# Performance work log

Hardware: AMD Instinct MI355X
Metric: run time of the kernel (lower is better)

Reference implementation:

```python
import jax, jax.numpy as jnp
import numpy as np

B, L, W = 4096, 30, 5          # batch, MAX_TOKEN_LENGTH, WINDOW_SIZE
A, E = 30, 128                 # ALPHABET_SIZE, embedding dim
C = 40                         # OUT_CHANNELS
H, T = 128, 3                  # LSTM_UNITS, num CRF tags
LIN = W * C                    # 200
EPS = 1e-5


def setup_inputs():
    key = jax.random.key(0)
    ks = jax.random.split(key, 24)
    def rn(k, shape, s=0.1):
        return jax.random.normal(k, shape, jnp.float32) * s
    return {
        'x': jax.random.randint(ks[0], (B, L, W), 0, A, jnp.int32),
        'emb': rn(ks[1], (A, E), 1.0),
        'conv_w': rn(ks[2], (C, E, 3)),
        'conv_b': rn(ks[3], (C,)),
        'bn1_g': 1.0 + rn(ks[4], (C,)),
        'bn1_b': rn(ks[5], (C,)),
        'bn1_m': rn(ks[6], (C,)),
        'bn1_v': 0.5 + jax.random.uniform(ks[7], (C,), jnp.float32),
        'w_ih_f': rn(ks[8], (4 * H, LIN)),
        'w_hh_f': rn(ks[9], (4 * H, H)),
        'b_f': rn(ks[10], (4 * H,)),
        'w_ih_b': rn(ks[11], (4 * H, LIN)),
        'w_hh_b': rn(ks[12], (4 * H, H)),
        'b_b': rn(ks[13], (4 * H,)),
        'bn2_g': 1.0 + rn(ks[14], (2 * H,)),
        'bn2_b': rn(ks[15], (2 * H,)),
        'bn2_m': rn(ks[16], (2 * H,)),
        'bn2_v': 0.5 + jax.random.uniform(ks[17], (2 * H,), jnp.float32),
        'fc_w': rn(ks[18], (T, 2 * H)),
        'fc_b': rn(ks[19], (T,)),
        'trans': rn(ks[20], (T, T)),
        'start_t': rn(ks[21], (T,)),
        'end_t': rn(ks[22], (T,)),
    }


def _lstm_dir(seq, w_ih, w_hh, b, reverse):
    # seq: [B, L, F]; torch gate order i, f, g, o
    xs = jnp.einsum('blf,gf->lbg', seq, w_ih) + b  # [L, B, 4H]
    h0 = jnp.zeros((seq.shape[0], H), seq.dtype)
    def step(carry, xt):
        h, c = carry
        z = xt + h @ w_hh.T
        i, f, g, o = jnp.split(z, 4, axis=-1)
        c = jax.nn.sigmoid(f) * c + jax.nn.sigmoid(i) * jnp.tanh(g)
        h = jax.nn.sigmoid(o) * jnp.tanh(c)
        return (h, c), h
    _, hs = jax.lax.scan(step, (h0, h0), xs, reverse=reverse)
    return hs.transpose(1, 0, 2)  # [B, L, H]


def _viterbi(emis, mask, trans, start_t, end_t):
    # emis: [B, L, T], mask: [B, L] bool
    score = start_t + emis[:, 0]                      # [B, T]
    def step(score, inp):
        e_t, m_t = inp                                # [B, T], [B]
        cand = score[:, :, None] + trans              # [B, Tprev, Tnext]
        ptr = jnp.argmax(cand, axis=1)                # [B, T]
        new = jnp.max(cand, axis=1) + e_t
        return jnp.where(m_t[:, None], new, score), ptr
    score, hist = jax.lax.scan(
        step, score, (emis[:, 1:].transpose(1, 0, 2), mask[:, 1:].T))
    score = score + end_t
    best = jnp.max(score, axis=1)                     # [B] path scores
    last = jnp.argmax(score, axis=1)                  # [B]
    def back(tag, inp):
        h_t, m_t = inp
        prev = jnp.take_along_axis(h_t, tag[:, None], axis=1)[:, 0]
        tag = jnp.where(m_t, prev, tag)
        return tag, tag
    _, ys = jax.lax.scan(back, last, (hist, mask[:, 1:].T), reverse=True)
    tags = jnp.concatenate([ys, last[None]], axis=0).T  # [B, L]
    return best, tags


def reference(x, emb, conv_w, conv_b, bn1_g, bn1_b, bn1_m, bn1_v,
              w_ih_f, w_hh_f, b_f, w_ih_b, w_hh_b, b_b,
              bn2_g, bn2_b, bn2_m, bn2_v, fc_w, fc_b, trans, start_t, end_t):
    mask = x[:, :, 2] > 0                             # [B, L]
    e = emb[x.reshape(B * L, W)]                      # [N, W, E]  (dropout=eval noop)
    e = e.transpose(0, 2, 1)                          # [N, E, W]
    y = jax.lax.conv_general_dilated(
        e, conv_w, (1,), [(1, 1)],
        dimension_numbers=('NCH', 'OIH', 'NCH')) + conv_b[:, None]
    # BatchNorm1d (inference, running stats)
    y = (y - bn1_m[:, None]) * (bn1_g / jnp.sqrt(bn1_v + EPS))[:, None] + bn1_b[:, None]
    y = jax.nn.relu(y)
    # MaxPool1d(k=3, stride=1, pad=1): length preserved
    y = jax.lax.reduce_window(y, -jnp.inf, jax.lax.max,
                              (1, 1, 3), (1, 1, 1),
                              [(0, 0), (0, 0), (1, 1)])
    y = y.reshape(B, L, LIN)                          # torch.flatten is channel-major = row-major reshape
    hf = _lstm_dir(y, w_ih_f, w_hh_f, b_f, False)
    hb = _lstm_dir(y, w_ih_b, w_hh_b, b_b, True)
    h = jnp.concatenate([hf, hb], axis=-1)            # [B, L, 2H]
    h = (h - bn2_m) * (bn2_g / jnp.sqrt(bn2_v + EPS)) + bn2_b
    emis = h @ fc_w.T + fc_b                          # [B, L, T]
    return _viterbi(emis, mask, trans, start_t, end_t)
```

## Files before the change

kernel.cpp:

```cpp
#include <hip/hip_runtime.h>
#include <math.h>

#define BB    4096
#define LL    30
#define WW    5
#define CC    40
#define HH    128
#define TT    3
#define KA    328
#define NB    32
#define NT_   512
#define FSTR  232
#define HSTR  136
#define CW    1056

#define WS_P    0
#define WS_BC   3600
#define WS_BG   3648
#define WS_WFC  4672
#define WS_EB   5440
#define WS_WBF  5504
#define WS_EMIS (5504 + 540672)

typedef __bf16 bf16x8 __attribute__((ext_vector_type(8)));
typedef float  f32x4  __attribute__((ext_vector_type(4)));
typedef unsigned short u16x8 __attribute__((ext_vector_type(8)));

__device__ __forceinline__ float sigm(float x) {
    return __builtin_amdgcn_rcpf(1.0f + __expf(-x));
}
__device__ __forceinline__ float tanh_fast(float x) {
    return 2.0f * __builtin_amdgcn_rcpf(1.0f + __expf(-2.0f * x)) - 1.0f;
}
__device__ __forceinline__ unsigned short f2bf(float f) {
    unsigned u = __builtin_bit_cast(unsigned, f);
    return (unsigned short)((u + 0x7FFFu + ((u >> 16) & 1u)) >> 16);
}
__device__ __forceinline__ float bf2f(unsigned short h) {
    unsigned u = ((unsigned)h) << 16;
    return __builtin_bit_cast(float, u);
}

__global__ void prep_kernel(const float* __restrict__ emb, const float* __restrict__ conv_w,
                            const float* __restrict__ conv_b,
                            const float* __restrict__ bn1_g, const float* __restrict__ bn1_b,
                            const float* __restrict__ bn1_m, const float* __restrict__ bn1_v,
                            const float* __restrict__ w_ih_f, const float* __restrict__ w_hh_f,
                            const float* __restrict__ b_f,
                            const float* __restrict__ w_ih_b, const float* __restrict__ w_hh_b,
                            const float* __restrict__ b_b,
                            const float* __restrict__ bn2_g, const float* __restrict__ bn2_b,
                            const float* __restrict__ bn2_m, const float* __restrict__ bn2_v,
                            const float* __restrict__ fc_w, const float* __restrict__ fc_b,
                            float* __restrict__ ws)
{
    const int gid = blockIdx.x * blockDim.x + threadIdx.x;
    const int gsz = gridDim.x * blockDim.x;

    for (int idx = gid; idx < 3600; idx += gsz) {
        int k = idx / 1200, rem = idx % 1200, a = rem / 40, c = rem % 40;
        float s1 = bn1_g[c] / sqrtf(bn1_v[c] + 1e-5f);
        float acc = 0.f;
        for (int e = 0; e < 128; ++e)
            acc += emb[a * 128 + e] * conv_w[(c * 128 + e) * 3 + k];
        ws[WS_P + idx] = acc * s1;
    }
    for (int c = gid; c < CC; c += gsz) {
        float s1 = bn1_g[c] / sqrtf(bn1_v[c] + 1e-5f);
        ws[WS_BC + c] = (conv_b[c] - bn1_m[c]) * s1 + bn1_b[c];
    }
    for (int i = gid; i < 1024; i += gsz) {
        int d = i >> 9, g = i & 511;
        ws[WS_BG + i] = d ? b_b[g] : b_f[g];
    }
    for (int i = gid; i < 768; i += gsz) {
        int d = i / 384, r = i % 384, t = r / 128, u = r % 128;
        int j = d * 128 + u;
        float s2 = bn2_g[j] / sqrtf(bn2_v[j] + 1e-5f);
        ws[WS_WFC + i] = fc_w[t * 256 + j] * s2;
    }
    for (int t = gid; t < TT; t += gsz) {
        float acc = fc_b[t];
        for (int j = 0; j < 256; ++j) {
            float s2 = bn2_g[j] / sqrtf(bn2_v[j] + 1e-5f);
            acc += fc_w[t * 256 + j] * (bn2_b[j] - bn2_m[j] * s2);
        }
        ws[WS_EB + t] = acc;
    }
    unsigned short* wsu = (unsigned short*)ws;
    for (int i = gid; i < 2 * 512 * CW; i += gsz) {
        int d = i / (512 * CW), r = i % (512 * CW);
        int n = r / CW, q = r % CW;
        int Ks = q / 96, t = q % 96, s = t / 32, k32 = t % 32;
        int k = Ks * 32 + k32;
        int u = n >> 2, g = n & 3, row = g * 128 + u;
        const float* wih = d ? w_ih_b : w_ih_f;
        const float* whh = d ? w_hh_b : w_hh_f;
        float w = (k < 200) ? wih[row * 200 + k]
                            : ((k >= 224) ? whh[row * 128 + (k - 224)] : 0.f);
        unsigned short t0 = f2bf(w);
        float r1 = w - bf2f(t0);
        unsigned short t1 = f2bf(r1);
        unsigned short t2 = f2bf(r1 - bf2f(t1));
        wsu[2 * WS_WBF + i] = (s == 0) ? t0 : ((s == 1) ? t1 : t2);
    }
}

__global__ __launch_bounds__(512, 2)
void lstm_kernel(const int* __restrict__ x, float* __restrict__ ws)
{
    __shared__ unsigned short Fh[2][NB * FSTR], Fl[2][NB * FSTR], Fm[2][NB * FSTR];
    __shared__ unsigned short Hh[2][NB * HSTR], Hl[2][NB * HSTR], Hm[2][NB * HSTR];
    __shared__ float Pp_s[3600];
    __shared__ float Wfc_s[384];
    __shared__ float biasC_s[40];

    const int tid = threadIdx.x;
    const int d   = blockIdx.x & 1;
    const int b0  = (blockIdx.x >> 1) * NB;

    const unsigned short* __restrict__ Wb =
        (const unsigned short*)ws + 2 * WS_WBF + d * (512 * CW);
    float* emis = ws + WS_EMIS + d * (BB * LL * TT);

    for (int i = tid; i < 3600; i += NT_) Pp_s[i] = ws[WS_P + i];
    for (int i = tid; i < 384;  i += NT_) Wfc_s[i] = ws[WS_WFC + d * 384 + i];
    for (int i = tid; i < 40;   i += NT_) biasC_s[i] = ws[WS_BC + i];
    for (int i = tid; i < NB * FSTR; i += NT_) {
        ((unsigned*)Fh)[i] = 0u; ((unsigned*)Fl)[i] = 0u; ((unsigned*)Fm)[i] = 0u;
    }
    for (int i = tid; i < NB * HSTR; i += NT_) {
        ((unsigned*)Hh)[i] = 0u; ((unsigned*)Hl)[i] = 0u; ((unsigned*)Hm)[i] = 0u;
    }

    const int lane = tid & 63;
    const int wv   = tid >> 6;
    const int quad = lane >> 4;
    const int ml   = lane & 15;
    const int skey = (wv ^ (wv >> 2)) & 1;

    const unsigned short* __restrict__ Wn[4] = {
        Wb + (wv * 64 +  0 + ml) * CW + quad * 8,
        Wb + (wv * 64 + 16 + ml) * CW + quad * 8,
        Wb + (wv * 64 + 32 + ml) * CW + quad * 8,
        Wb + (wv * 64 + 48 + ml) * CW + quad * 8
    };

    const float* bgp = ws + WS_BG + d * 512;
    int   un[4];
    float bIv[4], bFv[4], bGv[4], bOv[4];
    #pragma unroll
    for (int nt = 0; nt < 4; ++nt) {
        int u = wv * 16 + nt * 4 + quad;
        un[nt]  = u;
        bIv[nt] = bgp[u];
        bFv[nt] = bgp[128 + u];
        bGv[nt] = bgp[256 + u];
        bOv[nt] = bgp[384 + u];
    }

    float cst[2][4];
    #pragma unroll
    for (int mt = 0; mt < 2; ++mt)
        #pragma unroll
        for (int nt = 0; nt < 4; ++nt) cst[mt][nt] = 0.f;

    __syncthreads();

#define FEAT_ONE(LPOS, BUF, P)                                                 \
    {                                                                          \
        int bb = (P) / CC, c = (P) % CC;                                       \
        const int* tok = x + (((b0 + bb) * LL) + (LPOS)) * WW;                 \
        int t0 = tok[0], t1 = tok[1], t2 = tok[2], t3 = tok[3], t4 = tok[4];   \
        float bc = biasC_s[c];                                                 \
        float a0 = bc + Pp_s[(30 + t0) * 40 + c] + Pp_s[(60 + t1) * 40 + c];   \
        float a1 = bc + Pp_s[t0 * 40 + c] + Pp_s[(30 + t1) * 40 + c] + Pp_s[(60 + t2) * 40 + c]; \
        float a2 = bc + Pp_s[t1 * 40 + c] + Pp_s[(30 + t2) * 40 + c] + Pp_s[(60 + t3) * 40 + c]; \
        float a3 = bc + Pp_s[t2 * 40 + c] + Pp_s[(30 + t3) * 40 + c] + Pp_s[(60 + t4) * 40 + c]; \
        float a4 = bc + Pp_s[t3 * 40 + c] + Pp_s[(30 + t4) * 40 + c];          \
        a0 = fmaxf(a0, 0.f); a1 = fmaxf(a1, 0.f); a2 = fmaxf(a2, 0.f);         \
        a3 = fmaxf(a3, 0.f); a4 = fmaxf(a4, 0.f);                              \
        float f[5];                                                            \
        f[0] = fmaxf(a0, a1);                                                  \
        f[1] = fmaxf(fmaxf(a0, a1), a2);                                       \
        f[2] = fmaxf(fmaxf(a1, a2), a3);                                       \
        f[3] = fmaxf(fmaxf(a2, a3), a4);                                       \
        f[4] = fmaxf(a3, a4);                                                  \
        int base = bb * FSTR + c * 5;                                          \
        _Pragma("unroll")                                                      \
        for (int j = 0; j < 5; ++j) {                                          \
            unsigned short h0 = f2bf(f[j]);                                    \
            float r1 = f[j] - bf2f(h0);                                        \
            unsigned short h1 = f2bf(r1);                                      \
            unsigned short h2 = f2bf(r1 - bf2f(h1));                           \
            Fh[BUF][base + j] = h0;                                            \
            Fl[BUF][base + j] = h1;                                            \
            Fm[BUF][base + j] = h2;                                            \
        }                                                                      \
    }

#define FEAT_ITEMS(LPOS, BUF)                                                  \
    {                                                                          \
        FEAT_ONE(LPOS, BUF, tid)                                               \
        if (tid >= 192) FEAT_ONE(LPOS, BUF, tid + 320)                         \
        if (tid >= 192) FEAT_ONE(LPOS, BUF, tid + 640)                         \
        if (tid >= 384) FEAT_ONE(LPOS, BUF, tid + 768)                         \
    }

#define EMIS_BODY(LPOS, HB)                                                    \
    {                                                                          \
        int bb = tid / 6, r6 = tid % 6, t = r6 >> 1, seg = r6 & 1;             \
        int hoff = bb * HSTR + seg * 64;                                       \
        const float* wfc = &Wfc_s[t * 128 + seg * 64];                         \
        float s = 0.f;                                                         \
        _Pragma("unroll")                                                      \
        for (int i = 0; i < 8; ++i) {                                          \
            u16x8 v0 = *(const u16x8*)&Hh[HB][hoff + i * 8];                   \
            u16x8 v1 = *(const u16x8*)&Hl[HB][hoff + i * 8];                   \
            u16x8 v2 = *(const u16x8*)&Hm[HB][hoff + i * 8];                   \
            _Pragma("unroll")                                                  \
            for (int j = 0; j < 8; ++j) {                                      \
                float h = bf2f(v0[j]) + bf2f(v1[j]) + bf2f(v2[j]);             \
                s += h * wfc[i * 8 + j];                                       \
            }                                                                  \
        }                                                                      \
        s += __shfl_xor(s, 1);                                                 \
        if (seg == 0)                                                          \
            emis[(((b0 + bb) * LL) + (LPOS)) * TT + t] = s;                    \
    }

#define SHADOW_WORK(STEP_, FBN)                                                \
    {                                                                          \
        if ((STEP_) + 1 < LL) {                                                \
            const int lnext = d ? (LL - 2 - (STEP_)) : ((STEP_) + 1);          \
            FEAT_ITEMS(lnext, FBN)                                             \
        }                                                                      \
        if ((STEP_) > 0 && tid < 192) {                                        \
            const int lprev = d ? (LL - (STEP_)) : ((STEP_) - 1);              \
            EMIS_BODY(lprev, hr)                                               \
        }                                                                      \
    }

    {
        const int l0 = d ? (LL - 1) : 0;
        FEAT_ITEMS(l0, 0)
    }

#define WLOAD(B, P, KS)                                                        \
        {                                                                      \
            B[0] = *(const bf16x8*)((P) + (KS) * 96);                          \
            B[1] = *(const bf16x8*)((P) + (KS) * 96 + 32);                     \
            B[2] = *(const bf16x8*)((P) + (KS) * 96 + 64);                     \
        }
#define LDA(BUF, KS)                                                           \
        {                                                                      \
            if ((KS) < 7) {                                                    \
                const int ko_ = (KS) * 32 + quad * 8;                          \
                ah[BUF][0] = *(const bf16x8*)&Fh[fb][ml * FSTR + ko_];         \
                al[BUF][0] = *(const bf16x8*)&Fl[fb][ml * FSTR + ko_];         \
                am[BUF][0] = *(const bf16x8*)&Fm[fb][ml * FSTR + ko_];         \
                ah[BUF][1] = *(const bf16x8*)&Fh[fb][(16 + ml) * FSTR + ko_];  \
                al[BUF][1] = *(const bf16x8*)&Fl[fb][(16 + ml) * FSTR + ko_];  \
                am[BUF][1] = *(const bf16x8*)&Fm[fb][(16 + ml) * FSTR + ko_];  \
            } else {                                                           \
                const int ko_ = ((KS) - 7) * 32 + quad * 8;                    \
                ah[BUF][0] = *(const bf16x8*)&Hh[hr][ml * HSTR + ko_];         \
                al[BUF][0] = *(const bf16x8*)&Hl[hr][ml * HSTR + ko_];         \
                am[BUF][0] = *(const bf16x8*)&Hm[hr][ml * HSTR + ko_];         \
                ah[BUF][1] = *(const bf16x8*)&Hh[hr][(16 + ml) * HSTR + ko_];  \
                al[BUF][1] = *(const bf16x8*)&Hl[hr][(16 + ml) * HSTR + ko_];  \
                am[BUF][1] = *(const bf16x8*)&Hm[hr][(16 + ml) * HSTR + ko_];  \
            }                                                                  \
        }
#define GEMM6X(B, CB, NT)                                                      \
        {                                                                      \
            acc[0][NT] = __builtin_amdgcn_mfma_f32_16x16x32_bf16(B[0], ah[CB][0], acc[0][NT], 0, 0, 0); \
            acc[0][NT] = __builtin_amdgcn_mfma_f32_16x16x32_bf16(B[0], al[CB][0], acc[0][NT], 0, 0, 0); \
            acc[0][NT] = __builtin_amdgcn_mfma_f32_16x16x32_bf16(B[1], ah[CB][0], acc[0][NT], 0, 0, 0); \
            acc[0][NT] = __builtin_amdgcn_mfma_f32_16x16x32_bf16(B[1], al[CB][0], acc[0][NT], 0, 0, 0); \
            acc[0][NT] = __builtin_amdgcn_mfma_f32_16x16x32_bf16(B[2], ah[CB][0], acc[0][NT], 0, 0, 0); \
            acc[0][NT] = __builtin_amdgcn_mfma_f32_16x16x32_bf16(B[0], am[CB][0], acc[0][NT], 0, 0, 0); \
            acc[1][NT] = __builtin_amdgcn_mfma_f32_16x16x32_bf16(B[0], ah[CB][1], acc[1][NT], 0, 0, 0); \
            acc[1][NT] = __builtin_amdgcn_mfma_f32_16x16x32_bf16(B[0], al[CB][1], acc[1][NT], 0, 0, 0); \
            acc[1][NT] = __builtin_amdgcn_mfma_f32_16x16x32_bf16(B[1], ah[CB][1], acc[1][NT], 0, 0, 0); \
            acc[1][NT] = __builtin_amdgcn_mfma_f32_16x16x32_bf16(B[1], al[CB][1], acc[1][NT], 0, 0, 0); \
            acc[1][NT] = __builtin_amdgcn_mfma_f32_16x16x32_bf16(B[2], ah[CB][1], acc[1][NT], 0, 0, 0); \
            acc[1][NT] = __builtin_amdgcn_mfma_f32_16x16x32_bf16(B[0], am[CB][1], acc[1][NT], 0, 0, 0); \
        }
#define GATES_NT(NT)                                                           \
        {                                                                      \
            _Pragma("unroll")                                                  \
            for (int mt = 0; mt < 2; ++mt) {                                   \
                float zi = acc[mt][NT][0] + bIv[NT];                           \
                float zf = acc[mt][NT][1] + bFv[NT];                           \
                float zg = acc[mt][NT][2] + bGv[NT];                           \
                float zo = acc[mt][NT][3] + bOv[NT];                           \
                float cn = sigm(zf) * cst[mt][NT] + sigm(zi) * tanh_fast(zg);  \
                cst[mt][NT] = cn;                                              \
                float h = sigm(zo) * tanh_fast(cn);                            \
                unsigned short h0 = f2bf(h);                                   \
                float r1 = h - bf2f(h0);                                       \
                unsigned short h1 = f2bf(r1);                                  \
                unsigned short h2 = f2bf(r1 - bf2f(h1));                       \
                int idx = (mt * 16 + ml) * HSTR + un[NT];                      \
                Hh[hw][idx] = h0; Hl[hw][idx] = h1; Hm[hw][idx] = h2;          \
            }                                                                  \
        }

    bf16x8 wX[2][3], wY[2][3];
    WLOAD(wX[0], Wn[0], 0)
    WLOAD(wX[1], Wn[1], 0)

    __syncthreads();

    for (int step = 0; step < LL; ++step) {
        const int fb = step & 1;
        const int hw = step & 1;
        const int hr = hw ^ 1;

        f32x4 acc[2][4];
        #pragma unroll
        for (int mt = 0; mt < 2; ++mt)
            #pragma unroll
            for (int nt = 0; nt < 4; ++nt)
                acc[mt][nt] = (f32x4){0.f, 0.f, 0.f, 0.f};

        {
            bf16x8 ah[2][2], al[2][2], am[2][2];
            LDA(0, 0)

            #pragma unroll
            for (int Ks = 0; Ks < 10; ++Ks) {
                const int cb = Ks & 1, nb = cb ^ 1;

                WLOAD(wY[0], Wn[2], Ks)
                WLOAD(wY[1], Wn[3], Ks)
                LDA(nb, Ks + 1)

                __builtin_amdgcn_s_setprio(1);
                GEMM6X(wX[0], cb, 0)
                GEMM6X(wX[1], cb, 1)
                __builtin_amdgcn_s_setprio(0);

                WLOAD(wX[0], Wn[0], Ks + 1)
                WLOAD(wX[1], Wn[1], Ks + 1)
                __builtin_amdgcn_s_setprio(1);
                GEMM6X(wY[0], cb, 2)
                GEMM6X(wY[1], cb, 3)
                __builtin_amdgcn_s_setprio(0);

                if (Ks == 3 && skey == 0) SHADOW_WORK(step, fb ^ 1)
                if (Ks == 7 && skey == 1) SHADOW_WORK(step, fb ^ 1)
            }

            WLOAD(wY[0], Wn[2], 10)
            WLOAD(wY[1], Wn[3], 10)

            __builtin_amdgcn_s_setprio(1);
            GEMM6X(wX[0], 0, 0)
            GEMM6X(wX[1], 0, 1)
            __builtin_amdgcn_s_setprio(0);

            if (step + 1 < LL) {
                WLOAD(wX[0], Wn[0], 0)
                WLOAD(wX[1], Wn[1], 0)
            }
            GATES_NT(0)
            GATES_NT(1)

            __builtin_amdgcn_s_setprio(1);
            GEMM6X(wY[0], 0, 2)
            GEMM6X(wY[1], 0, 3)
            __builtin_amdgcn_s_setprio(0);

            GATES_NT(2)
            GATES_NT(3)
        }

        __syncthreads();
    }
#undef GATES_NT
#undef GEMM6X
#undef LDA
#undef WLOAD

    if (tid < 192) {
        const int llast = d ? 0 : (LL - 1);
        const int hl_ = (LL - 1) & 1;
        EMIS_BODY(llast, hl_)
    }
#undef SHADOW_WORK
#undef EMIS_BODY
#undef FEAT_ITEMS
#undef FEAT_ONE
}

__global__ void viterbi_kernel(const int* __restrict__ x, const float* __restrict__ ws,
                               const float* __restrict__ trans,
                               const float* __restrict__ start_t,
                               const float* __restrict__ end_t,
                               float* __restrict__ out)
{
    int b = blockIdx.x * blockDim.x + threadIdx.x;
    if (b >= BB) return;
    const float* eF = ws + WS_EMIS;
    const float* eB = ws + WS_EMIS + BB * LL * TT;
    const float eb0 = ws[WS_EB + 0], eb1 = ws[WS_EB + 1], eb2 = ws[WS_EB + 2];
    float tr[9];
    #pragma unroll
    for (int i = 0; i < 9; ++i) tr[i] = trans[i];

    int base = b * LL * TT;
    float s0 = start_t[0] + eF[base + 0] + eB[base + 0] + eb0;
    float s1 = start_t[1] + eF[base + 1] + eB[base + 1] + eb1;
    float s2 = start_t[2] + eF[base + 2] + eB[base + 2] + eb2;

    unsigned hist[LL - 1];
    unsigned maskbits = 0;

    #pragma unroll
    for (int l = 1; l < LL; ++l) {
        bool m = x[(b * LL + l) * WW + 2] > 0;
        if (m) maskbits |= (1u << l);
        int idx = base + l * TT;
        float e0 = eF[idx + 0] + eB[idx + 0] + eb0;
        float e1 = eF[idx + 1] + eB[idx + 1] + eb1;
        float e2 = eF[idx + 2] + eB[idx + 2] + eb2;

        float ns[3]; int pt[3];
        #pragma unroll
        for (int nt = 0; nt < 3; ++nt) {
            float c0 = s0 + tr[0 * 3 + nt];
            float c1 = s1 + tr[1 * 3 + nt];
            float c2 = s2 + tr[2 * 3 + nt];
            int p = 0; float bc = c0;
            if (c1 > bc) { bc = c1; p = 1; }
            if (c2 > bc) { bc = c2; p = 2; }
            ns[nt] = bc; pt[nt] = p;
        }
        ns[0] += e0; ns[1] += e1; ns[2] += e2;
        hist[l - 1] = (unsigned)pt[0] | ((unsigned)pt[1] << 2) | ((unsigned)pt[2] << 4);
        if (m) { s0 = ns[0]; s1 = ns[1]; s2 = ns[2]; }
    }
    s0 += end_t[0]; s1 += end_t[1]; s2 += end_t[2];
    float best = s0; int last = 0;
    if (s1 > best) { best = s1; last = 1; }
    if (s2 > best) { best = s2; last = 2; }

    out[b] = best;
    float* tags = out + BB + b * LL;
    int tag = last;
    tags[LL - 1] = (float)last;
    #pragma unroll
    for (int l = LL - 1; l >= 1; --l) {
        int prev = (int)((hist[l - 1] >> (2 * tag)) & 3u);
        if (maskbits & (1u << l)) tag = prev;
        tags[l - 1] = (float)tag;
    }
}

extern "C" void kernel_launch(void* const* d_in, const int* in_sizes, int n_in,
                              void* d_out, int out_size, void* d_ws, size_t ws_size,
                              hipStream_t stream)
{
    const int*   x      = (const int*)  d_in[0];
    const float* emb    = (const float*)d_in[1];
    const float* conv_w = (const float*)d_in[2];
    const float* conv_b = (const float*)d_in[3];
    const float* bn1_g  = (const float*)d_in[4];
    const float* bn1_b  = (const float*)d_in[5];
    const float* bn1_m  = (const float*)d_in[6];
    const float* bn1_v  = (const float*)d_in[7];
    const float* w_ih_f = (const float*)d_in[8];
    const float* w_hh_f = (const float*)d_in[9];
    const float* b_f    = (const float*)d_in[10];
    const float* w_ih_b = (const float*)d_in[11];
    const float* w_hh_b = (const float*)d_in[12];
    const float* b_b    = (const float*)d_in[13];
    const float* bn2_g  = (const float*)d_in[14];
    const float* bn2_b  = (const float*)d_in[15];
    const float* bn2_m  = (const float*)d_in[16];
    const float* bn2_v  = (const float*)d_in[17];
    const float* fc_w   = (const float*)d_in[18];
    const float* fc_b   = (const float*)d_in[19];
    const float* trans  = (const float*)d_in[20];
    const float* start_t= (const float*)d_in[21];
    const float* end_t  = (const float*)d_in[22];

    float* ws  = (float*)d_ws;
    float* out = (float*)d_out;

    prep_kernel<<<256, 256, 0, stream>>>(emb, conv_w, conv_b,
                                         bn1_g, bn1_b, bn1_m, bn1_v,
                                         w_ih_f, w_hh_f, b_f,
                                         w_ih_b, w_hh_b, b_b,
                                         bn2_g, bn2_b, bn2_m, bn2_v,
                                         fc_w, fc_b, ws);
    lstm_kernel<<<256, 512, 0, stream>>>(x, ws);
    viterbi_kernel<<<16, 256, 0, stream>>>(x, ws, trans, start_t, end_t, out);
}
```

Baseline: 721.6 us.

## Spread LSTM gate tiles over 12 waves with uneven light/heavy work split

```diff
diff --git a/kernel.cpp b/kernel.cpp
--- a/kernel.cpp
+++ b/kernel.cpp
@@ -9,7 +9,7 @@
 #define TT    3
 #define KA    328
 #define NB    32
-#define NT_   512
+#define NT_   768
 #define FSTR  232
 #define HSTR  136
 #define CW    1056
@@ -106,7 +106,7 @@
     }
 }
 
-__global__ __launch_bounds__(512, 2)
+__global__ __launch_bounds__(768, 3)
 void lstm_kernel(const int* __restrict__ x, float* __restrict__ ws)
 {
     __shared__ unsigned short Fh[2][NB * FSTR], Fl[2][NB * FSTR], Fm[2][NB * FSTR];
@@ -137,21 +137,31 @@
     const int wv   = tid >> 6;
     const int quad = lane >> 4;
     const int ml   = lane & 15;
-    const int skey = (wv ^ (wv >> 2)) & 1;
-
-    const unsigned short* __restrict__ Wn[4] = {
-        Wb + (wv * 64 +  0 + ml) * CW + quad * 8,
-        Wb + (wv * 64 + 16 + ml) * CW + quad * 8,
-        Wb + (wv * 64 + 32 + ml) * CW + quad * 8,
-        Wb + (wv * 64 + 48 + ml) * CW + quad * 8
-    };
+
+    const int lightw = (wv == 2) | (wv == 3) | (wv == 8) | (wv == 9);
+    const int tb4 = (wv == 0) ? 0 : (wv == 1) ? 12 : (wv == 2) ? 24 :
+                    (wv == 3) ? 32 : (wv == 4) ? 40 : (wv == 5) ? 52 :
+                    (wv == 6) ? 64 : (wv == 7) ? 76 : (wv == 8) ? 88 :
+                    (wv == 9) ? 96 : (wv == 10) ? 104 : 116;
+    const int cb0 = tb4 * 4;
+    const int fb0 = (wv == 0) ? 0 : (wv == 1) ? 64 : (wv == 2) ? 128 :
+                    (wv == 3) ? 320 : (wv == 4) ? 512 : (wv == 5) ? 576 :
+                    (wv == 6) ? 640 : (wv == 7) ? 704 : (wv == 8) ? 768 :
+                    (wv == 9) ? 960 : (wv == 10) ? 1152 : 1216;
+    const int it0 = fb0 + lane;
+
+    const unsigned short* __restrict__ Wt[3];
+    Wt[0] = Wb + (cb0 +  0 + ml) * CW + quad * 8;
+    Wt[1] = Wb + (cb0 + 16 + ml) * CW + quad * 8;
+    Wt[2] = lightw ? Wt[0] : (Wb + (cb0 + 32 + ml) * CW + quad * 8);
 
     const float* bgp = ws + WS_BG + d * 512;
-    int   un[4];
-    float bIv[4], bFv[4], bGv[4], bOv[4];
+    int   un[3];
+    float bIv[3], bFv[3], bGv[3], bOv[3];
     #pragma unroll
-    for (int nt = 0; nt < 4; ++nt) {
-        int u = wv * 16 + nt * 4 + quad;
+    for (int nt = 0; nt < 3; ++nt) {
+        int u = tb4 + nt * 4 + quad;
+        u = (u > 127) ? 127 : u;
         un[nt]  = u;
         bIv[nt] = bgp[u];
         bFv[nt] = bgp[128 + u];
@@ -159,11 +169,11 @@
         bOv[nt] = bgp[384 + u];
     }
 
-    float cst[2][4];
+    float cst[2][3];
     #pragma unroll
     for (int mt = 0; mt < 2; ++mt)
         #pragma unroll
-        for (int nt = 0; nt < 4; ++nt) cst[mt][nt] = 0.f;
+        for (int nt = 0; nt < 3; ++nt) cst[mt][nt] = 0.f;
 
     __syncthreads();
 
@@ -199,17 +209,9 @@
         }                                                                      \
     }
 
-#define FEAT_ITEMS(LPOS, BUF)                                                  \
+#define EMIS_BODY(LPOS, HB, PIDX)                                              \
     {                                                                          \
-        FEAT_ONE(LPOS, BUF, tid)                                               \
-        if (tid >= 192) FEAT_ONE(LPOS, BUF, tid + 320)                         \
-        if (tid >= 192) FEAT_ONE(LPOS, BUF, tid + 640)                         \
-        if (tid >= 384) FEAT_ONE(LPOS, BUF, tid + 768)                         \
-    }
-
-#define EMIS_BODY(LPOS, HB)                                                    \
-    {                                                                          \
-        int bb = tid / 6, r6 = tid % 6, t = r6 >> 1, seg = r6 & 1;             \
+        int bb = (PIDX) / 6, r6 = (PIDX) % 6, t = r6 >> 1, seg = r6 & 1;       \
         int hoff = bb * HSTR + seg * 64;                                       \
         const float* wfc = &Wfc_s[t * 128 + seg * 64];                         \
         float s = 0.f;                                                         \
@@ -229,24 +231,7 @@
             emis[(((b0 + bb) * LL) + (LPOS)) * TT + t] = s;                    \
     }
 
-#define SHADOW_WORK(STEP_, FBN)                                                \
-    {                                                                          \
-        if ((STEP_) + 1 < LL) {                                                \
-            const int lnext = d ? (LL - 2 - (STEP_)) : ((STEP_) + 1);          \
-            FEAT_ITEMS(lnext, FBN)                                             \
-        }                                                                      \
-        if ((STEP_) > 0 && tid < 192) {                                        \
-            const int lprev = d ? (LL - (STEP_)) : ((STEP_) - 1);              \
-            EMIS_BODY(lprev, hr)                                               \
-        }                                                                      \
-    }
-
-    {
-        const int l0 = d ? (LL - 1) : 0;
-        FEAT_ITEMS(l0, 0)
-    }
-
-#define WLOAD(B, P, KS)                                                        \
+#define WLOADT(B, P, KS)                                                       \
         {                                                                      \
             B[0] = *(const bf16x8*)((P) + (KS) * 96);                          \
             B[1] = *(const bf16x8*)((P) + (KS) * 96 + 32);                     \
@@ -307,9 +292,19 @@
             }                                                                  \
         }
 
-    bf16x8 wX[2][3], wY[2][3];
-    WLOAD(wX[0], Wn[0], 0)
-    WLOAD(wX[1], Wn[1], 0)
+    {
+        const int l0 = d ? (LL - 1) : 0;
+        if (!lightw) {
+            FEAT_ONE(l0, 0, it0)
+        } else {
+            FEAT_ONE(l0, 0, it0)
+            FEAT_ONE(l0, 0, it0 + 64)
+            FEAT_ONE(l0, 0, it0 + 128)
+        }
+    }
+
+    bf16x8 wb[2][3];
+    WLOADT(wb[0], Wt[0], 0)
 
     __syncthreads();
 
@@ -318,63 +313,115 @@
         const int hw = step & 1;
         const int hr = hw ^ 1;
 
-        f32x4 acc[2][4];
-        #pragma unroll
-        for (int mt = 0; mt < 2; ++mt)
+        f32x4 acc[2][3];
+
+        if (!lightw) {
             #pragma unroll
-            for (int nt = 0; nt < 4; ++nt)
-                acc[mt][nt] = (f32x4){0.f, 0.f, 0.f, 0.f};
-
-        {
+            for (int mt = 0; mt < 2; ++mt)
+                #pragma unroll
+                for (int nt = 0; nt < 3; ++nt)
+                    acc[mt][nt] = (f32x4){0.f, 0.f, 0.f, 0.f};
+
             bf16x8 ah[2][2], al[2][2], am[2][2];
             LDA(0, 0)
 
             #pragma unroll
-            for (int Ks = 0; Ks < 10; ++Ks) {
+            for (int Ks = 0; Ks < 11; ++Ks) {
                 const int cb = Ks & 1, nb = cb ^ 1;
 
-                WLOAD(wY[0], Wn[2], Ks)
-                WLOAD(wY[1], Wn[3], Ks)
-                LDA(nb, Ks + 1)
+                WLOADT(wb[nb], Wt[1], Ks)
+                if (Ks < 10) LDA(nb, Ks + 1)
 
                 __builtin_amdgcn_s_setprio(1);
-                GEMM6X(wX[0], cb, 0)
-                GEMM6X(wX[1], cb, 1)
+                GEMM6X(wb[cb], cb, 0)
                 __builtin_amdgcn_s_setprio(0);
 
-                WLOAD(wX[0], Wn[0], Ks + 1)
-                WLOAD(wX[1], Wn[1], Ks + 1)
+                WLOADT(wb[cb], Wt[2], Ks)
+
                 __builtin_amdgcn_s_setprio(1);
-                GEMM6X(wY[0], cb, 2)
-                GEMM6X(wY[1], cb, 3)
+                GEMM6X(wb[nb], cb, 1)
                 __builtin_amdgcn_s_setprio(0);
 
-                if (Ks == 3 && skey == 0) SHADOW_WORK(step, fb ^ 1)
-                if (Ks == 7 && skey == 1) SHADOW_WORK(step, fb ^ 1)
+                if (Ks < 10) WLOADT(wb[nb], Wt[0], Ks + 1)
+
+                __builtin_amdgcn_s_setprio(1);
+                GEMM6X(wb[cb], cb, 2)
+                __builtin_amdgcn_s_setprio(0);
+
+                if (Ks == 3 && step + 1 < LL && (wv & 3) == 0) {
+                    const int ln = d ? (LL - 2 - step) : (step + 1);
+                    FEAT_ONE(ln, fb ^ 1, it0)
+                }
+                if (Ks == 5 && step + 1 < LL && (wv & 3) == 1) {
+                    const int ln = d ? (LL - 2 - step) : (step + 1);
+                    FEAT_ONE(ln, fb ^ 1, it0)
+                }
+                if (Ks == 7 && step + 1 < LL && (wv & 3) == 2) {
+                    const int ln = d ? (LL - 2 - step) : (step + 1);
+                    FEAT_ONE(ln, fb ^ 1, it0)
+                }
+                if (Ks == 9 && step + 1 < LL && (wv & 3) == 3) {
+                    const int ln = d ? (LL - 2 - step) : (step + 1);
+                    FEAT_ONE(ln, fb ^ 1, it0)
+                }
             }
 
-            WLOAD(wY[0], Wn[2], 10)
-            WLOAD(wY[1], Wn[3], 10)
-
-            __builtin_amdgcn_s_setprio(1);
-            GEMM6X(wX[0], 0, 0)
-            GEMM6X(wX[1], 0, 1)
-            __builtin_amdgcn_s_setprio(0);
-
-            if (step + 1 < LL) {
-                WLOAD(wX[0], Wn[0], 0)
-                WLOAD(wX[1], Wn[1], 0)
-            }
             GATES_NT(0)
             GATES_NT(1)
-
-            __builtin_amdgcn_s_setprio(1);
-            GEMM6X(wY[0], 0, 2)
-            GEMM6X(wY[1], 0, 3)
-            __builtin_amdgcn_s_setprio(0);
-
             GATES_NT(2)
-            GATES_NT(3)
+
+            if (step + 1 < LL) WLOADT(wb[0], Wt[0], 0)
+        } else {
+            #pragma unroll
+            for (int mt = 0; mt < 2; ++mt)
+                #pragma unroll
+                for (int nt = 0; nt < 2; ++nt)
+                    acc[mt][nt] = (f32x4){0.f, 0.f, 0.f, 0.f};
+
+            bf16x8 ah[2][2], al[2][2], am[2][2];
+            LDA(0, 0)
+
+            #pragma unroll
+            for (int Ks = 0; Ks < 11; ++Ks) {
+                const int cb = Ks & 1, nb = cb ^ 1;
+
+                WLOADT(wb[1], Wt[1], Ks)
+                if (Ks < 10) LDA(nb, Ks + 1)
+
+                __builtin_amdgcn_s_setprio(1);
+                GEMM6X(wb[0], cb, 0)
+                __builtin_amdgcn_s_setprio(0);
+
+                if (Ks < 10) WLOADT(wb[0], Wt[0], Ks + 1)
+
+                __builtin_amdgcn_s_setprio(1);
+                GEMM6X(wb[1], cb, 1)
+                __builtin_amdgcn_s_setprio(0);
+
+                if (Ks == 2 && step + 1 < LL) {
+                    const int ln = d ? (LL - 2 - step) : (step + 1);
+                    FEAT_ONE(ln, fb ^ 1, it0)
+                }
+                if (Ks == 5 && step + 1 < LL) {
+                    const int ln = d ? (LL - 2 - step) : (step + 1);
+                    FEAT_ONE(ln, fb ^ 1, it0 + 64)
+                }
+                if (Ks == 8 && step + 1 < LL) {
+                    const int ln = d ? (LL - 2 - step) : (step + 1);
+                    FEAT_ONE(ln, fb ^ 1, it0 + 128)
+                }
+            }
+
+            if (step > 0 && wv != 9) {
+                const int lprev = d ? (LL - step) : (step - 1);
+                const int p = (wv == 8) ? (tid - 384) : (tid - 128);
+                EMIS_BODY(lprev, hr, p)
+            }
+
+            GATES_NT(0)
+            GATES_NT(1)
+
+            if (step + 1 < LL) WLOADT(wb[0], Wt[0], 0)
         }
 
         __syncthreads();
@@ -382,16 +429,15 @@
 #undef GATES_NT
 #undef GEMM6X
 #undef LDA
-#undef WLOAD
-
-    if (tid < 192) {
+#undef WLOADT
+
+    if (lightw && wv != 9) {
         const int llast = d ? 0 : (LL - 1);
         const int hl_ = (LL - 1) & 1;
-        EMIS_BODY(llast, hl_)
-    }
-#undef SHADOW_WORK
+        const int p = (wv == 8) ? (tid - 384) : (tid - 128);
+        EMIS_BODY(llast, hl_, p)
+    }
 #undef EMIS_BODY
-#undef FEAT_ITEMS
 #undef FEAT_ONE
 }
 
@@ -496,6 +542,6 @@
                                          w_ih_b, w_hh_b, b_b,
                                          bn2_g, bn2_b, bn2_m, bn2_v,
                                          fc_w, fc_b, ws);
-    lstm_kernel<<<256, 512, 0, stream>>>(x, ws);
+    lstm_kernel<<<256, 768, 0, stream>>>(x, ws);
     viterbi_kernel<<<16, 256, 0, stream>>>(x, ws, trans, start_t, end_t, out);
 }
```

After: 760.7 us. +5.4%, slower.
